# Optimization experiments

Measured on AMD Instinct MI355X. Metric: run time of the kernel, lower is better.

Reference implementation:

```python
import jax, jax.numpy as jnp
import numpy as np

N = 50000          # nodes
E = 800000         # edges (avg degree 16)
IN, HID, OUT = 128, 128, 32
BN_EPS = 1e-5


def gcn_conv(x, W, b, src, dst):
    """PyG GCNConv: D^-1/2 (A+I) D^-1/2 (x @ W) + b, self-loops included."""
    h = x @ W                                                  # [N, out]
    ones = jnp.ones((src.shape[0],), dtype=x.dtype)
    deg = jax.ops.segment_sum(ones, dst, num_segments=N) + 1.0  # in-degree + self-loop
    dis = jax.lax.rsqrt(deg)                                    # deg^-1/2
    norm = dis[src] * dis[dst]                                  # [E]
    msg = h[src] * norm[:, None]                                # gather + scale, [E, out]
    agg = jax.ops.segment_sum(msg, dst, num_segments=N)         # scatter-add
    agg = agg + h * (dis * dis)[:, None]                        # self-loop term (norm = 1/deg_i)
    return agg + b


def bn_relu(h, g, be):
    # BatchNorm1d in training mode: batch statistics over the node dimension
    mu = jnp.mean(h, axis=0)
    var = jnp.mean((h - mu) ** 2, axis=0)  # biased variance, as torch BN
    return jax.nn.relu((h - mu) * jax.lax.rsqrt(var + BN_EPS) * g + be)


def setup_inputs() -> dict:
    key = jax.random.key(0)
    ks = jax.random.split(key, 8)
    x = jax.random.normal(ks[0], (N, IN), dtype=jnp.float32)
    edge_index = jax.random.randint(ks[1], (2, E), 0, N, dtype=jnp.int64)
    W0 = jax.random.normal(ks[2], (IN, HID), dtype=jnp.float32) / np.sqrt(IN)
    W1 = jax.random.normal(ks[3], (HID, HID), dtype=jnp.float32) / np.sqrt(HID)
    W2 = jax.random.normal(ks[4], (HID, OUT), dtype=jnp.float32) / np.sqrt(HID)
    return {
        "x": x, "edge_index": edge_index,
        "W0": W0, "b0": jnp.zeros((HID,), jnp.float32),
        "g0": jnp.ones((HID,), jnp.float32), "be0": jnp.zeros((HID,), jnp.float32),
        "W1": W1, "b1": jnp.zeros((HID,), jnp.float32),
        "g1": jnp.ones((HID,), jnp.float32), "be1": jnp.zeros((HID,), jnp.float32),
        "W2": W2, "b2": jnp.zeros((OUT,), jnp.float32),
    }


def reference(x, edge_index, W0, b0, g0, be0, W1, b1, g1, be1, W2, b2):
    src, dst = edge_index[0], edge_index[1]
    # block 0: conv -> BN -> ReLU -> (dropout: eval, identity) -> residual
    h = bn_relu(gcn_conv(x, W0, b0, src, dst), g0, be0)
    x = h + x  # use_residual, in_channels == hidden, res_proj is None
    # block 1
    h = bn_relu(gcn_conv(x, W1, b1, src, dst), g1, be1)
    x = h + x
    # final conv + log_softmax over classes
    out = gcn_conv(x, W2, b2, src, dst)
    return jax.nn.log_softmax(out, axis=1)
```

## Files before the change

### kernel.cpp

```cpp
#include <hip/hip_runtime.h>
#include <math.h>

#define NN 50000
#define NNP (NN + 1)
#define NE 800000
#define NEP 1150000
#define NBLK 49
#define NBKT 7
#define BCAP 262144
#define GEMMBLK 782
#define FILLBLK 512

typedef __attribute__((ext_vector_type(8))) short short8;
typedef __attribute__((ext_vector_type(4))) float float4v;

__device__ inline unsigned int f2bf(float f) {
  unsigned int u = __float_as_uint(f);
  return (u + 0x7fffu + ((u >> 16) & 1u)) >> 16;
}
__device__ inline unsigned int pack2bf(float lo, float hi) {
  return f2bf(lo) | (f2bf(hi) << 16);
}
__device__ inline float bflo(unsigned int p) { return __uint_as_float(p << 16); }
__device__ inline float bfhi(unsigned int p) { return __uint_as_float(p & 0xffff0000u); }

__device__ inline void bn_fold(const float* __restrict__ gstat, const float* __restrict__ g,
                               const float* __restrict__ be, float* __restrict__ bnabS, int tid) {
  if (tid < 128) {
    float s = 0.f, q = 0.f;
    #pragma unroll
    for (int r = 0; r < 8; r++) {
      s += gstat[r * 256 + tid];
      q += gstat[r * 256 + 128 + tid];
    }
    const float inv = 1.f / (float)NN;
    float m = s * inv;
    float var = q * inv - m * m;
    float a = rsqrtf(var + 1e-5f) * g[tid];
    bnabS[tid] = a;
    bnabS[128 + tid] = be[tid] - m * a;
  }
}


__global__ __launch_bounds__(256) void k_init(int* __restrict__ deg, float* __restrict__ gstat,
                                              int* __restrict__ binCnt,
                                              const float* __restrict__ W0, const float* __restrict__ W1,
                                              const float* __restrict__ W2,
                                              unsigned short* __restrict__ wt16) {
  int i = blockIdx.x * 256 + threadIdx.x;
  if (i < NN) deg[i] = 0;
  if (i < 4096) gstat[i] = 0.f;
  if (i < NBKT) binCnt[i] = 0;
  if (i < 32768) {
    int w = i >> 14;
    int rem = i & 16383;
    int k = rem >> 7;
    int n = rem & 127;
    const float* W = w ? W1 : W0;
    wt16[w * 16384 + n * 128 + k] = (unsigned short)f2bf(W[k * 128 + n]);
  } else if (i < 36864) {
    int idx = i - 32768;
    int n = idx >> 7;
    int k = idx & 127;
    wt16[32768 + n * 128 + k] = (unsigned short)f2bf(W2[k * 32 + n]);
  }
}


__global__ __launch_bounds__(1024) void k_binA(const int* __restrict__ src, const int* __restrict__ dst,
                                               int* __restrict__ deg, int* __restrict__ binCnt,
                                               int2* __restrict__ bin) {
  __shared__ int lcnt[NBKT], lbase[NBKT];
  int tid = threadIdx.x;
  if (tid < NBKT) lcnt[tid] = 0;
  __syncthreads();
  int e = blockIdx.x * 1024 + tid;
  bool act = e < NE;
  int d = 0, s = 0, b = 0, rank = 0, drank = 0;
  if (act) {
    d = dst[e]; s = src[e];
    b = d >> 13;
    drank = atomicAdd(&deg[d], 1);
    rank = atomicAdd(&lcnt[b], 1);
  }
  __syncthreads();
  if (tid < NBKT && lcnt[tid] > 0) lbase[tid] = atomicAdd(&binCnt[tid], lcnt[tid]);
  __syncthreads();
  if (act) bin[(size_t)b * BCAP + lbase[b] + rank] =
      make_int2((int)((unsigned)d | ((unsigned)drank << 16)), s);
}


__global__ __launch_bounds__(1024) void k_scan1(const int* __restrict__ deg, int* __restrict__ degtot,
                                                int* __restrict__ excl, int* __restrict__ blksum) {
  __shared__ int smW[16];
  int t = threadIdx.x;
  int i = blockIdx.x * 1024 + t;
  int wv = t >> 6, ln = t & 63;
  int tot = 0;
  if (i < NN) {
    tot = deg[i];
    degtot[i] = tot;
  }
  int v = (i < NN) ? ((tot + 7) & ~7) : 0;
  int sc = v;
  #pragma unroll
  for (int off = 1; off < 64; off <<= 1) {
    int u = __shfl_up(sc, off);
    if (ln >= off) sc += u;
  }
  if (ln == 63) smW[wv] = sc;
  __syncthreads();
  if (t < 64) {
    int wsum = (t < 16) ? smW[t] : 0;
    int s2 = wsum;
    #pragma unroll
    for (int off = 1; off < 16; off <<= 1) {
      int u = __shfl_up(s2, off);
      if (t >= off) s2 += u;
    }
    if (t < 16) smW[t] = s2 - wsum;
    if (t == 15) blksum[blockIdx.x] = s2;
  }
  __syncthreads();
  if (i < NN) excl[i] = (sc - v) + smW[wv];
}


__global__ __launch_bounds__(256) void k_scan3(int* __restrict__ rowstart, const int* __restrict__ blksum,
                                               const int* __restrict__ degtot,
                                               float* __restrict__ dis,
                                               unsigned short* __restrict__ hs16, float* __restrict__ h2) {
  __shared__ int offS;
  int tid = threadIdx.x;
  int i = blockIdx.x * 256 + tid;
  int myblk = blockIdx.x >> 2;
  if (tid < 64) {
    int bv = (tid < NBLK) ? blksum[tid] : 0;
    int sc = bv;
    #pragma unroll
    for (int off = 1; off < 64; off <<= 1) {
      int u = __shfl_up(sc, off);
      if (tid >= off) sc += u;
    }
    int pre = (myblk > 0) ? __shfl(sc, myblk - 1) : 0;
    int total = __shfl(sc, NBLK - 1);
    if (tid == 0) {
      offS = pre;
      if (blockIdx.x == 0) rowstart[NN] = total;
    }
  }
  __syncthreads();
  int boff = offS;
  if (i < NN) {
    rowstart[i] = rowstart[i] + boff;
    dis[i] = rsqrtf((float)degtot[i] + 1.0f);
  }
  if (i < 64) {
    int slice = i >> 5, c = i & 31;
    ((unsigned int*)(hs16 + (size_t)slice * ((size_t)NNP * 64) + (size_t)NN * 64))[c] = 0u;
  }
  if (i < 32) h2[(size_t)NN * 32 + i] = 0.f;
}


__global__ __launch_bounds__(256) void k_fillgemm(const int2* __restrict__ bin,
                                                  const int* __restrict__ binCnt,
                                                  const int* __restrict__ rowstart,
                                                  int* __restrict__ csr_src,
                                                  const float* __restrict__ X,
                                                  const unsigned short* __restrict__ Wt,
                                                  const float* __restrict__ dis,
                                                  unsigned short* __restrict__ hs16) {
  __shared__ char smem[52224];
  const int tid = threadIdx.x;

  if (blockIdx.x < FILLBLK) {
    int bb = blockIdx.x;
    int b = bb & 7;
    if (b >= NBKT) return;
    int q = bb >> 3;
    int cnt = binCnt[b];
    const int2* __restrict__ B = bin + (size_t)b * BCAP;
    for (int i = q * 256 + tid; i < cnt; i += 64 * 256) {
      int2 ds = B[i];
      unsigned int v = (unsigned int)ds.x;
      int d = (int)(v & 0xffffu);
      int rank = (int)(v >> 16);
      csr_src[rowstart[d] + rank] = ds.y;
    }
    return;
  }

  unsigned short* A  = (unsigned short*)smem;
  unsigned short* Bt = (unsigned short*)(smem + 17408);
  float* C = (float*)smem;
  const int row0 = (blockIdx.x - FILLBLK) * 64;
  const int M = NN;

  {
    int c4 = tid & 31;
    #pragma unroll
    for (int i = 0; i < 8; i++) {
      int r = (tid >> 5) + i * 8;
      int gr = row0 + r;
      float4 v = make_float4(0.f, 0.f, 0.f, 0.f);
      if (gr < M) v = *(const float4*)(X + (size_t)gr * 128 + c4 * 4);
      *(uint2*)(A + r * 136 + c4 * 4) = make_uint2(pack2bf(v.x, v.y), pack2bf(v.z, v.w));
    }
  }
  {
    int r = tid >> 1, h = (tid & 1) * 64;
    const uint4* src = (const uint4*)(Wt + r * 128 + h);
    uint4* dst = (uint4*)(Bt + r * 136 + h);
    #pragma unroll
    for (int i = 0; i < 8; i++) dst[i] = src[i];
  }
  __syncthreads();

  const int wv = tid >> 6;
  const int l = tid & 63;
  const int lm = l & 15;
  const int lq = l >> 4;

  float4v acc[8];
  #pragma unroll
  for (int j = 0; j < 8; j++) acc[j] = (float4v)(0.f);

  const unsigned short* Arow = A + (wv * 16 + lm) * 136 + lq * 8;
  #pragma unroll
  for (int ks = 0; ks < 4; ks++) {
    short8 af = *(const short8*)(Arow + ks * 32);
    #pragma unroll
    for (int j = 0; j < 8; j++) {
      short8 bf = *(const short8*)(Bt + (j * 16 + lm) * 136 + lq * 8 + ks * 32);
      acc[j] = __builtin_amdgcn_mfma_f32_16x16x32_bf16(af, bf, acc[j], 0, 0, 0);
    }
  }
  __syncthreads();

  #pragma unroll
  for (int j = 0; j < 8; j++) {
    int col = j * 16 + lm;
    int rbase = wv * 16 + lq * 4;
    #pragma unroll
    for (int r = 0; r < 4; r++) C[(rbase + r) * 132 + col] = acc[j][r];
  }
  __syncthreads();

  {
    #pragma unroll
    for (int i = 0; i < 4; i++) {
      int idx = tid + i * 256;
      int slice = idx >> 9;
      int r = (idx >> 3) & 63;
      int ch = idx & 7;
      int gr = row0 + r;
      if (gr < M) {
        float d = dis[gr];
        const float* cp = C + r * 132 + slice * 64 + ch * 8;
        uint4 u;
        u.x = pack2bf(cp[0] * d, cp[1] * d);
        u.y = pack2bf(cp[2] * d, cp[3] * d);
        u.z = pack2bf(cp[4] * d, cp[5] * d);
        u.w = pack2bf(cp[6] * d, cp[7] * d);
        *(uint4*)(hs16 + (size_t)slice * ((size_t)NNP * 64) + (size_t)gr * 64 + ch * 8) = u;
      }
    }
  }
}


__global__ __launch_bounds__(256) void k_gemm128f(const unsigned short* __restrict__ O16,
                                                  const float* __restrict__ Xin,
                                                  unsigned short* __restrict__ XA16,
                                                  const float* __restrict__ gstat,
                                                  const float* __restrict__ g,
                                                  const float* __restrict__ be,
                                                  const unsigned short* __restrict__ Wt,
                                                  const float* __restrict__ dis,
                                                  unsigned short* __restrict__ hs16, int M) {
  __shared__ char smem[52224];
  __shared__ float bnabS[256];
  unsigned short* A  = (unsigned short*)smem;
  unsigned short* Bt = (unsigned short*)(smem + 17408);
  float* C = (float*)smem;
  const int tid = threadIdx.x;
  const int row0 = blockIdx.x * 64;

  bn_fold(gstat, g, be, bnabS, tid);
  __syncthreads();

  {
    int c = tid & 15;
    float4 alo = *(const float4*)(bnabS + c * 8);
    float4 ahi = *(const float4*)(bnabS + c * 8 + 4);
    float4 clo = *(const float4*)(bnabS + 128 + c * 8);
    float4 chi = *(const float4*)(bnabS + 128 + c * 8 + 4);
    #pragma unroll
    for (int i = 0; i < 4; i++) {
      int r = (tid >> 4) + i * 16;
      int gr = row0 + r;
      uint4 u = make_uint4(0u, 0u, 0u, 0u);
      if (gr < M) {
        uint4 ou = *(const uint4*)(O16 + (size_t)gr * 128 + c * 8);
        float4 xlo = *(const float4*)(Xin + (size_t)gr * 128 + c * 8);
        float4 xhi = *(const float4*)(Xin + (size_t)gr * 128 + c * 8 + 4);
        float v0 = fmaxf(bflo(ou.x) * alo.x + clo.x, 0.f) + xlo.x;
        float v1 = fmaxf(bfhi(ou.x) * alo.y + clo.y, 0.f) + xlo.y;
        float v2 = fmaxf(bflo(ou.y) * alo.z + clo.z, 0.f) + xlo.z;
        float v3 = fmaxf(bfhi(ou.y) * alo.w + clo.w, 0.f) + xlo.w;
        float v4 = fmaxf(bflo(ou.z) * ahi.x + chi.x, 0.f) + xhi.x;
        float v5 = fmaxf(bfhi(ou.z) * ahi.y + chi.y, 0.f) + xhi.y;
        float v6 = fmaxf(bflo(ou.w) * ahi.z + chi.z, 0.f) + xhi.z;
        float v7 = fmaxf(bfhi(ou.w) * ahi.w + chi.w, 0.f) + xhi.w;
        u.x = pack2bf(v0, v1);
        u.y = pack2bf(v2, v3);
        u.z = pack2bf(v4, v5);
        u.w = pack2bf(v6, v7);
        *(uint4*)(XA16 + (size_t)gr * 128 + c * 8) = u;
      }
      *(uint4*)(A + r * 136 + c * 8) = u;
    }
  }
  {
    int r = tid >> 1, h = (tid & 1) * 64;
    const uint4* src = (const uint4*)(Wt + r * 128 + h);
    uint4* dst = (uint4*)(Bt + r * 136 + h);
    #pragma unroll
    for (int i = 0; i < 8; i++) dst[i] = src[i];
  }
  __syncthreads();

  const int wv = tid >> 6;
  const int l = tid & 63;
  const int lm = l & 15;
  const int lq = l >> 4;

  float4v acc[8];
  #pragma unroll
  for (int j = 0; j < 8; j++) acc[j] = (float4v)(0.f);

  const unsigned short* Arow = A + (wv * 16 + lm) * 136 + lq * 8;
  #pragma unroll
  for (int ks = 0; ks < 4; ks++) {
    short8 af = *(const short8*)(Arow + ks * 32);
    #pragma unroll
    for (int j = 0; j < 8; j++) {
      short8 bf = *(const short8*)(Bt + (j * 16 + lm) * 136 + lq * 8 + ks * 32);
      acc[j] = __builtin_amdgcn_mfma_f32_16x16x32_bf16(af, bf, acc[j], 0, 0, 0);
    }
  }
  __syncthreads();

  #pragma unroll
  for (int j = 0; j < 8; j++) {
    int col = j * 16 + lm;
    int rbase = wv * 16 + lq * 4;
    #pragma unroll
    for (int r = 0; r < 4; r++) C[(rbase + r) * 132 + col] = acc[j][r];
  }
  __syncthreads();

  {
    #pragma unroll
    for (int i = 0; i < 4; i++) {
      int idx = tid + i * 256;
      int slice = idx >> 9;
      int r = (idx >> 3) & 63;
      int ch = idx & 7;
      int gr = row0 + r;
      if (gr < M) {
        float d = dis[gr];
        const float* cp = C + r * 132 + slice * 64 + ch * 8;
        uint4 u;
        u.x = pack2bf(cp[0] * d, cp[1] * d);
        u.y = pack2bf(cp[2] * d, cp[3] * d);
        u.z = pack2bf(cp[4] * d, cp[5] * d);
        u.w = pack2bf(cp[6] * d, cp[7] * d);
        *(uint4*)(hs16 + (size_t)slice * ((size_t)NNP * 64) + (size_t)gr * 64 + ch * 8) = u;
      }
    }
  }
}


__global__ __launch_bounds__(256) void k_gemm32mf(const unsigned short* __restrict__ O16,
                                                  const unsigned short* __restrict__ XA16,
                                                  const float* __restrict__ gstat,
                                                  const float* __restrict__ g,
                                                  const float* __restrict__ be,
                                                  const unsigned short* __restrict__ Wt2,
                                                  const float* __restrict__ dis,
                                                  float* __restrict__ H, int M) {
  __shared__ char smem[26112];
  __shared__ float bnabS[256];
  unsigned short* A   = (unsigned short*)smem;
  unsigned short* Bt2 = (unsigned short*)(smem + 17408);
  float* C = (float*)smem;
  const int tid = threadIdx.x;
  const int row0 = blockIdx.x * 64;

  bn_fold(gstat, g, be, bnabS, tid);
  __syncthreads();

  {
    int c = tid & 15;
    float4 alo = *(const float4*)(bnabS + c * 8);
    float4 ahi = *(const float4*)(bnabS + c * 8 + 4);
    float4 clo = *(const float4*)(bnabS + 128 + c * 8);
    float4 chi = *(const float4*)(bnabS + 128 + c * 8 + 4);
    #pragma unroll
    for (int i = 0; i < 4; i++) {
      int r = (tid >> 4) + i * 16;
      int gr = row0 + r;
      uint4 u = make_uint4(0u, 0u, 0u, 0u);
      if (gr < M) {
        uint4 ou = *(const uint4*)(O16 + (size_t)gr * 128 + c * 8);
        uint4 xu = *(const uint4*)(XA16 + (size_t)gr * 128 + c * 8);
        float v0 = fmaxf(bflo(ou.x) * alo.x + clo.x, 0.f) + bflo(xu.x);
        float v1 = fmaxf(bfhi(ou.x) * alo.y + clo.y, 0.f) + bfhi(xu.x);
        float v2 = fmaxf(bflo(ou.y) * alo.z + clo.z, 0.f) + bflo(xu.y);
        float v3 = fmaxf(bfhi(ou.y) * alo.w + clo.w, 0.f) + bfhi(xu.y);
        float v4 = fmaxf(bflo(ou.z) * ahi.x + chi.x, 0.f) + bflo(xu.z);
        float v5 = fmaxf(bfhi(ou.z) * ahi.y + chi.y, 0.f) + bfhi(xu.z);
        float v6 = fmaxf(bflo(ou.w) * ahi.z + chi.z, 0.f) + bflo(xu.w);
        float v7 = fmaxf(bfhi(ou.w) * ahi.w + chi.w, 0.f) + bfhi(xu.w);
        u.x = pack2bf(v0, v1);
        u.y = pack2bf(v2, v3);
        u.z = pack2bf(v4, v5);
        u.w = pack2bf(v6, v7);
      }
      *(uint4*)(A + r * 136 + c * 8) = u;
    }
  }
  {
    int r = tid >> 3, h = (tid & 7) * 16;
    const uint4* src = (const uint4*)(Wt2 + r * 128 + h);
    uint4* dst = (uint4*)(Bt2 + r * 136 + h);
    dst[0] = src[0];
    dst[1] = src[1];
  }
  __syncthreads();

  const int wv = tid >> 6;
  const int l = tid & 63;
  const int lm = l & 15;
  const int lq = l >> 4;

  float4v acc[2];
  acc[0] = (float4v)(0.f);
  acc[1] = (float4v)(0.f);

  const unsigned short* Arow = A + (wv * 16 + lm) * 136 + lq * 8;
  #pragma unroll
  for (int ks = 0; ks < 4; ks++) {
    short8 af = *(const short8*)(Arow + ks * 32);
    #pragma unroll
    for (int j = 0; j < 2; j++) {
      short8 bf = *(const short8*)(Bt2 + (j * 16 + lm) * 136 + lq * 8 + ks * 32);
      acc[j] = __builtin_amdgcn_mfma_f32_16x16x32_bf16(af, bf, acc[j], 0, 0, 0);
    }
  }
  __syncthreads();

  #pragma unroll
  for (int j = 0; j < 2; j++) {
    int col = j * 16 + lm;
    int rbase = wv * 16 + lq * 4;
    #pragma unroll
    for (int r = 0; r < 4; r++) C[(rbase + r) * 36 + col] = acc[j][r];
  }
  __syncthreads();

  {
    #pragma unroll
    for (int i = 0; i < 2; i++) {
      int idx = tid + i * 256;
      int r = idx >> 3;
      int ch = idx & 7;
      int gr = row0 + r;
      if (gr < M) {
        float d = dis[gr];
        const float* cp = C + r * 36 + ch * 4;
        float4 v = make_float4(cp[0] * d, cp[1] * d, cp[2] * d, cp[3] * d);
        *(float4*)(H + (size_t)gr * 32 + ch * 4) = v;
      }
    }
  }
}


__global__ __launch_bounds__(256) void k_agg128s(const unsigned short* __restrict__ Hs,
                                                 const float* __restrict__ dis,
                                                 const int* __restrict__ rowstart,
                                                 const int* __restrict__ degtot,
                                                 const int* __restrict__ csr_src,
                                                 const float* __restrict__ bias,
                                                 unsigned short* __restrict__ out16,
                                                 float* __restrict__ gstat) {
  __shared__ float smS[4][128], smQ[4][128];
  const int tid = threadIdx.x;
  const int wv = tid >> 6;
  const int lane = tid & 63;
  const int node_sub = lane >> 3;
  const int fl = lane & 7;
  const int base = node_sub * 8;
  const int w = blockIdx.x * 32 + wv * 8 + node_sub;
  const bool act = w < NN;
  const unsigned short* __restrict__ S0 = Hs + fl * 8;
  const unsigned short* __restrict__ S1 = Hs + (size_t)NNP * 64 + fl * 8;
  float di = act ? dis[w] : 0.f;
  int e0 = 0, e1 = 0, dend = 0;
  if (act) { e0 = rowstart[w]; e1 = rowstart[w + 1]; dend = e0 + degtot[w]; }

  float a0[8], a1[8];
  #pragma unroll
  for (int j = 0; j < 8; j++) { a0[j] = 0.f; a1[j] = 0.f; }

  int idxCur = (e0 < e1) ? csr_src[e0 + fl] : 0;
  for (int e = e0; e < e1; e += 8) {
    int cur = (e + fl < dend) ? idxCur : (int)NN;
    if (e + 8 < e1) idxCur = csr_src[e + 8 + fl];
    int s0 = __shfl(cur, base + 0), s1 = __shfl(cur, base + 1);
    int s2 = __shfl(cur, base + 2), s3 = __shfl(cur, base + 3);
    int s4 = __shfl(cur, base + 4), s5 = __shfl(cur, base + 5);
    int s6 = __shfl(cur, base + 6), s7 = __shfl(cur, base + 7);
    uint4 g0 = *(const uint4*)(S0 + (size_t)s0 * 64);
    uint4 g1 = *(const uint4*)(S0 + (size_t)s1 * 64);
    uint4 g2 = *(const uint4*)(S0 + (size_t)s2 * 64);
    uint4 g3 = *(const uint4*)(S0 + (size_t)s3 * 64);
    uint4 g4 = *(const uint4*)(S0 + (size_t)s4 * 64);
    uint4 g5 = *(const uint4*)(S0 + (size_t)s5 * 64);
    uint4 g6 = *(const uint4*)(S0 + (size_t)s6 * 64);
    uint4 g7 = *(const uint4*)(S0 + (size_t)s7 * 64);
    uint4 h0 = *(const uint4*)(S1 + (size_t)s0 * 64);
    uint4 h1 = *(const uint4*)(S1 + (size_t)s1 * 64);
    uint4 h2 = *(const uint4*)(S1 + (size_t)s2 * 64);
    uint4 h3 = *(const uint4*)(S1 + (size_t)s3 * 64);
    uint4 h4 = *(const uint4*)(S1 + (size_t)s4 * 64);
    uint4 h5 = *(const uint4*)(S1 + (size_t)s5 * 64);
    uint4 h6 = *(const uint4*)(S1 + (size_t)s6 * 64);
    uint4 h7 = *(const uint4*)(S1 + (size_t)s7 * 64);
    a0[0] += ((bflo(g0.x) + bflo(g1.x)) + (bflo(g2.x) + bflo(g3.x))) + ((bflo(g4.x) + bflo(g5.x)) + (bflo(g6.x) + bflo(g7.x)));
    a0[1] += ((bfhi(g0.x) + bfhi(g1.x)) + (bfhi(g2.x) + bfhi(g3.x))) + ((bfhi(g4.x) + bfhi(g5.x)) + (bfhi(g6.x) + bfhi(g7.x)));
    a0[2] += ((bflo(g0.y) + bflo(g1.y)) + (bflo(g2.y) + bflo(g3.y))) + ((bflo(g4.y) + bflo(g5.y)) + (bflo(g6.y) + bflo(g7.y)));
    a0[3] += ((bfhi(g0.y) + bfhi(g1.y)) + (bfhi(g2.y) + bfhi(g3.y))) + ((bfhi(g4.y) + bfhi(g5.y)) + (bfhi(g6.y) + bfhi(g7.y)));
    a0[4] += ((bflo(g0.z) + bflo(g1.z)) + (bflo(g2.z) + bflo(g3.z))) + ((bflo(g4.z) + bflo(g5.z)) + (bflo(g6.z) + bflo(g7.z)));
    a0[5] += ((bfhi(g0.z) + bfhi(g1.z)) + (bfhi(g2.z) + bfhi(g3.z))) + ((bfhi(g4.z) + bfhi(g5.z)) + (bfhi(g6.z) + bfhi(g7.z)));
    a0[6] += ((bflo(g0.w) + bflo(g1.w)) + (bflo(g2.w) + bflo(g3.w))) + ((bflo(g4.w) + bflo(g5.w)) + (bflo(g6.w) + bflo(g7.w)));
    a0[7] += ((bfhi(g0.w) + bfhi(g1.w)) + (bfhi(g2.w) + bfhi(g3.w))) + ((bfhi(g4.w) + bfhi(g5.w)) + (bfhi(g6.w) + bfhi(g7.w)));
    a1[0] += ((bflo(h0.x) + bflo(h1.x)) + (bflo(h2.x) + bflo(h3.x))) + ((bflo(h4.x) + bflo(h5.x)) + (bflo(h6.x) + bflo(h7.x)));
    a1[1] += ((bfhi(h0.x) + bfhi(h1.x)) + (bfhi(h2.x) + bfhi(h3.x))) + ((bfhi(h4.x) + bfhi(h5.x)) + (bfhi(h6.x) + bfhi(h7.x)));
    a1[2] += ((bflo(h0.y) + bflo(h1.y)) + (bflo(h2.y) + bflo(h3.y))) + ((bflo(h4.y) + bflo(h5.y)) + (bflo(h6.y) + bflo(h7.y)));
    a1[3] += ((bfhi(h0.y) + bfhi(h1.y)) + (bfhi(h2.y) + bfhi(h3.y))) + ((bfhi(h4.y) + bfhi(h5.y)) + (bfhi(h6.y) + bfhi(h7.y)));
    a1[4] += ((bflo(h0.z) + bflo(h1.z)) + (bflo(h2.z) + bflo(h3.z))) + ((bflo(h4.z) + bflo(h5.z)) + (bflo(h6.z) + bflo(h7.z)));
    a1[5] += ((bfhi(h0.z) + bfhi(h1.z)) + (bfhi(h2.z) + bfhi(h3.z))) + ((bfhi(h4.z) + bfhi(h5.z)) + (bfhi(h6.z) + bfhi(h7.z)));
    a1[6] += ((bflo(h0.w) + bflo(h1.w)) + (bflo(h2.w) + bflo(h3.w))) + ((bflo(h4.w) + bflo(h5.w)) + (bflo(h6.w) + bflo(h7.w)));
    a1[7] += ((bfhi(h0.w) + bfhi(h1.w)) + (bfhi(h2.w) + bfhi(h3.w))) + ((bfhi(h4.w) + bfhi(h5.w)) + (bfhi(h6.w) + bfhi(h7.w)));
  }

  float rv0[8], rv1[8];
  if (act) {
    uint4 sv0 = *(const uint4*)(S0 + (size_t)w * 64);
    uint4 sv1 = *(const uint4*)(S1 + (size_t)w * 64);
    float se0[8] = { bflo(sv0.x), bfhi(sv0.x), bflo(sv0.y), bfhi(sv0.y),
                     bflo(sv0.z), bfhi(sv0.z), bflo(sv0.w), bfhi(sv0.w) };
    float se1[8] = { bflo(sv1.x), bfhi(sv1.x), bflo(sv1.y), bfhi(sv1.y),
                     bflo(sv1.z), bfhi(sv1.z), bflo(sv1.w), bfhi(sv1.w) };
    #pragma unroll
    for (int j = 0; j < 8; j++) {
      rv0[j] = (a0[j] + se0[j]) * di + bias[fl * 8 + j];
      rv1[j] = (a1[j] + se1[j]) * di + bias[64 + fl * 8 + j];
    }
    uint4 u0, u1;
    u0.x = pack2bf(rv0[0], rv0[1]); u0.y = pack2bf(rv0[2], rv0[3]);
    u0.z = pack2bf(rv0[4], rv0[5]); u0.w = pack2bf(rv0[6], rv0[7]);
    u1.x = pack2bf(rv1[0], rv1[1]); u1.y = pack2bf(rv1[2], rv1[3]);
    u1.z = pack2bf(rv1[4], rv1[5]); u1.w = pack2bf(rv1[6], rv1[7]);
    *(uint4*)(out16 + (size_t)w * 128 + fl * 8)      = u0;
    *(uint4*)(out16 + (size_t)w * 128 + 64 + fl * 8) = u1;
  } else {
    #pragma unroll
    for (int j = 0; j < 8; j++) { rv0[j] = 0.f; rv1[j] = 0.f; }
  }

  float q0[8], q1[8];
  #pragma unroll
  for (int j = 0; j < 8; j++) { q0[j] = rv0[j] * rv0[j]; q1[j] = rv1[j] * rv1[j]; }
  #pragma unroll
  for (int off = 8; off <= 32; off <<= 1) {
    #pragma unroll
    for (int j = 0; j < 8; j++) {
      rv0[j] += __shfl_xor(rv0[j], off);
      q0[j]  += __shfl_xor(q0[j], off);
      rv1[j] += __shfl_xor(rv1[j], off);
      q1[j]  += __shfl_xor(q1[j], off);
    }
  }
  if (node_sub == 0) {
    #pragma unroll
    for (int j = 0; j < 8; j++) {
      smS[wv][fl * 8 + j] = rv0[j];      smQ[wv][fl * 8 + j] = q0[j];
      smS[wv][64 + fl * 8 + j] = rv1[j]; smQ[wv][64 + fl * 8 + j] = q1[j];
    }
  }
  __syncthreads();
  if (tid < 128) {
    float s = (smS[0][tid] + smS[1][tid]) + (smS[2][tid] + smS[3][tid]);
    float q = (smQ[0][tid] + smQ[1][tid]) + (smQ[2][tid] + smQ[3][tid]);
    int rep = blockIdx.x & 7;
    atomicAdd(&gstat[rep * 256 + tid], s);
    atomicAdd(&gstat[rep * 256 + 128 + tid], q);
  }
}


__global__ __launch_bounds__(256) void k_agg32lsm(const float* __restrict__ H2,
                                                  const float* __restrict__ dis,
                                                  const int* __restrict__ rowstart,
                                                  const int* __restrict__ degtot,
                                                  const int* __restrict__ csr_src,
                                                  const float* __restrict__ bias,
                                                  float* __restrict__ out) {
  int wave = (blockIdx.x * 256 + threadIdx.x) >> 6;
  int lane = threadIdx.x & 63;
  int half = lane >> 5;
  int l = lane & 31;
  int hbase = half * 32;
  int w = wave * 2 + half;
  if (w >= NN) return;
  const float* __restrict__ S = H2 + l;
  float di = dis[w];
  int e0 = rowstart[w], e1 = rowstart[w + 1];
  int dend = e0 + degtot[w];
  float acc = 0.f;
  for (int e = e0; e < e1; e += 8) {
    int myIdx = csr_src[e + (l & 7)];
    if (e + (l & 7) >= dend) myIdx = NN;
    int s0 = __shfl(myIdx, hbase + 0), s1 = __shfl(myIdx, hbase + 1);
    int s2 = __shfl(myIdx, hbase + 2), s3 = __shfl(myIdx, hbase + 3);
    int s4 = __shfl(myIdx, hbase + 4), s5 = __shfl(myIdx, hbase + 5);
    int s6 = __shfl(myIdx, hbase + 6), s7 = __shfl(myIdx, hbase + 7);
    float h0 = S[(size_t)s0 * 32], h1 = S[(size_t)s1 * 32];
    float h2v = S[(size_t)s2 * 32], h3 = S[(size_t)s3 * 32];
    float h4 = S[(size_t)s4 * 32], h5 = S[(size_t)s5 * 32];
    float h6 = S[(size_t)s6 * 32], h7 = S[(size_t)s7 * 32];
    acc += ((h0 + h1) + (h2v + h3)) + ((h4 + h5) + (h6 + h7));
  }
  float v = (acc + S[(size_t)w * 32]) * di + bias[l];
  float m = v;
  #pragma unroll
  for (int off = 16; off >= 1; off >>= 1) m = fmaxf(m, __shfl_xor(m, off));
  float ex = expf(v - m);
  float s = ex;
  #pragma unroll
  for (int off = 16; off >= 1; off >>= 1) s += __shfl_xor(s, off);
  out[(size_t)w * 32 + l] = v - m - logf(s);
}


extern "C" void kernel_launch(void* const* d_in, const int* in_sizes, int n_in,
                              void* d_out, int out_size, void* d_ws, size_t ws_size,
                              hipStream_t stream) {
  const float* x   = (const float*)d_in[0];
  const int*   ei  = (const int*)d_in[1];
  const float* W0  = (const float*)d_in[2];
  const float* b0  = (const float*)d_in[3];
  const float* g0  = (const float*)d_in[4];
  const float* be0 = (const float*)d_in[5];
  const float* W1  = (const float*)d_in[6];
  const float* b1  = (const float*)d_in[7];
  const float* g1  = (const float*)d_in[8];
  const float* be1 = (const float*)d_in[9];
  const float* W2  = (const float*)d_in[10];
  const float* b2  = (const float*)d_in[11];
  float* out = (float*)d_out;
  const int* srcI = ei;
  const int* dstI = ei + NE;

  char* p = (char*)d_ws;
  auto take = [&](size_t bytes) { char* r = p; p += (bytes + 255) & ~(size_t)255; return (void*)r; };
  int*   deg      = (int*)take(NN * 4);
  int*   degtot   = (int*)take(NN * 4);
  int*   rowstart = (int*)take((NN + 1) * 4);
  int*   blksum   = (int*)take(64 * 4);
  int*   binCnt   = (int*)take(8 * 4);
  float* dis      = (float*)take(NN * 4);
  int*   csr      = (int*)take((size_t)NEP * 4);
  int2*  bin      = (int2*)take((size_t)NBKT * BCAP * 8);
  float* gstat    = (float*)take(4096 * 4);
  unsigned short* wt16 = (unsigned short*)take((2 * 16384 + 4096) * 2);
  unsigned short* hs16 = (unsigned short*)take((size_t)NNP * 128 * 2);
  unsigned short* o16  = (unsigned short*)take((size_t)NN * 128 * 2);
  unsigned short* xA16 = (unsigned short*)take((size_t)NN * 128 * 2);
  float* h2       = (float*)take((size_t)NNP * 32 * 4);

  k_init<<<(NN + 255) / 256, 256, 0, stream>>>(deg, gstat, binCnt, W0, W1, W2, wt16);
  k_binA<<<(NE + 1023) / 1024, 1024, 0, stream>>>(srcI, dstI, deg, binCnt, bin);
  k_scan1<<<NBLK, 1024, 0, stream>>>(deg, degtot, rowstart, blksum);
  k_scan3<<<(NN + 255) / 256, 256, 0, stream>>>(rowstart, blksum, degtot, dis, hs16, h2);

  const int aggGrid = (NN + 31) / 32;
  const int aggGrid32 = (NN + 7) / 8;

  k_fillgemm<<<FILLBLK + GEMMBLK, 256, 0, stream>>>(bin, binCnt, rowstart, csr, x, wt16, dis, hs16);
  k_agg128s<<<aggGrid, 256, 0, stream>>>(hs16, dis, rowstart, degtot, csr, b0, o16, gstat);

  k_gemm128f<<<(NN + 63) / 64, 256, 0, stream>>>(o16, x, xA16, gstat, g0, be0,
                                                 wt16 + 16384, dis, hs16, NN);
  k_agg128s<<<aggGrid, 256, 0, stream>>>(hs16, dis, rowstart, degtot, csr, b1, o16, gstat + 2048);

  k_gemm32mf<<<(NN + 63) / 64, 256, 0, stream>>>(o16, xA16, gstat + 2048, g1, be1,
                                                 wt16 + 32768, dis, h2, NN);
  k_agg32lsm<<<aggGrid32, 256, 0, stream>>>(h2, dis, rowstart, degtot, csr, b2, out);
}
```

Before: 259.2 us.

## Merge preprocessing kernels: memset init, fold weight convert into binning, single-pass scan

Replaces the init kernel with a hipMemsetAsync over one contiguous zeroed region and moves the weight bf16 transpose into the edge-binning kernel. The two scan kernels become a single kernel that uses a global atomic counter as a grid barrier across its 49 blocks before applying block offsets and computing dis. The fill partition is also rebalanced to 448 blocks using modulo 7 so no blocks idle. This cuts launch count and overhead, but the spin barrier assumes all 49 blocks are co-resident.

```diff
diff --git a/kernel.cpp b/kernel.cpp
--- a/kernel.cpp
+++ b/kernel.cpp
@@ -9,7 +9,7 @@
 #define NBKT 7
 #define BCAP 262144
 #define GEMMBLK 782
-#define FILLBLK 512
+#define FILLBLK 448
 
 typedef __attribute__((ext_vector_type(8))) short short8;
 typedef __attribute__((ext_vector_type(4))) float float4v;
@@ -43,37 +43,31 @@
 }
 
 
-__global__ __launch_bounds__(256) void k_init(int* __restrict__ deg, float* __restrict__ gstat,
-                                              int* __restrict__ binCnt,
-                                              const float* __restrict__ W0, const float* __restrict__ W1,
-                                              const float* __restrict__ W2,
-                                              unsigned short* __restrict__ wt16) {
-  int i = blockIdx.x * 256 + threadIdx.x;
-  if (i < NN) deg[i] = 0;
-  if (i < 4096) gstat[i] = 0.f;
-  if (i < NBKT) binCnt[i] = 0;
-  if (i < 32768) {
-    int w = i >> 14;
-    int rem = i & 16383;
+__global__ __launch_bounds__(1024) void k_binAW(const int* __restrict__ src, const int* __restrict__ dst,
+                                                int* __restrict__ deg, int* __restrict__ binCnt,
+                                                int2* __restrict__ bin,
+                                                const float* __restrict__ W0, const float* __restrict__ W1,
+                                                const float* __restrict__ W2,
+                                                unsigned short* __restrict__ wt16) {
+  __shared__ int lcnt[NBKT], lbase[NBKT];
+  int tid = threadIdx.x;
+  if (tid < NBKT) lcnt[tid] = 0;
+
+  int j = blockIdx.x * 1024 + tid;
+  if (j < 32768) {
+    int w = j >> 14;
+    int rem = j & 16383;
     int k = rem >> 7;
     int n = rem & 127;
     const float* W = w ? W1 : W0;
     wt16[w * 16384 + n * 128 + k] = (unsigned short)f2bf(W[k * 128 + n]);
-  } else if (i < 36864) {
-    int idx = i - 32768;
+  } else if (j < 36864) {
+    int idx = j - 32768;
     int n = idx >> 7;
     int k = idx & 127;
     wt16[32768 + n * 128 + k] = (unsigned short)f2bf(W2[k * 32 + n]);
   }
-}
-
-
-__global__ __launch_bounds__(1024) void k_binA(const int* __restrict__ src, const int* __restrict__ dst,
-                                               int* __restrict__ deg, int* __restrict__ binCnt,
-                                               int2* __restrict__ bin) {
-  __shared__ int lcnt[NBKT], lbase[NBKT];
-  int tid = threadIdx.x;
-  if (tid < NBKT) lcnt[tid] = 0;
+
   __syncthreads();
   int e = blockIdx.x * 1024 + tid;
   bool act = e < NE;
@@ -92,9 +86,13 @@
 }
 
 
-__global__ __launch_bounds__(1024) void k_scan1(const int* __restrict__ deg, int* __restrict__ degtot,
-                                                int* __restrict__ excl, int* __restrict__ blksum) {
+__global__ __launch_bounds__(1024) void k_scan(const int* __restrict__ deg, int* __restrict__ degtot,
+                                               int* __restrict__ rowstart, int* __restrict__ blksum,
+                                               int* __restrict__ syncCnt,
+                                               float* __restrict__ dis,
+                                               unsigned short* __restrict__ hs16, float* __restrict__ h2) {
   __shared__ int smW[16];
+  __shared__ int smB[2];
   int t = threadIdx.x;
   int i = blockIdx.x * 1024 + t;
   int wv = t >> 6, ln = t & 63;
@@ -121,47 +119,43 @@
       if (t >= off) s2 += u;
     }
     if (t < 16) smW[t] = s2 - wsum;
-    if (t == 15) blksum[blockIdx.x] = s2;
-  }
-  __syncthreads();
-  if (i < NN) excl[i] = (sc - v) + smW[wv];
-}
-
-
-__global__ __launch_bounds__(256) void k_scan3(int* __restrict__ rowstart, const int* __restrict__ blksum,
-                                               const int* __restrict__ degtot,
-                                               float* __restrict__ dis,
-                                               unsigned short* __restrict__ hs16, float* __restrict__ h2) {
-  __shared__ int offS;
-  int tid = threadIdx.x;
-  int i = blockIdx.x * 256 + tid;
-  int myblk = blockIdx.x >> 2;
-  if (tid < 64) {
-    int bv = (tid < NBLK) ? blksum[tid] : 0;
-    int sc = bv;
+    if (t == 15) atomicExch(&blksum[blockIdx.x], s2);
+  }
+  __syncthreads();
+  int excl = (sc - v) + smW[wv];
+
+  if (t == 0) {
+    atomicAdd(syncCnt, 1);
+    while (atomicAdd(syncCnt, 0) < NBLK) { }
+  }
+  __syncthreads();
+
+  if (t < 64) {
+    int bv = (t < NBLK) ? atomicAdd(&blksum[t], 0) : 0;
+    int sc2 = bv;
     #pragma unroll
     for (int off = 1; off < 64; off <<= 1) {
-      int u = __shfl_up(sc, off);
-      if (tid >= off) sc += u;
-    }
-    int pre = (myblk > 0) ? __shfl(sc, myblk - 1) : 0;
-    int total = __shfl(sc, NBLK - 1);
-    if (tid == 0) {
-      offS = pre;
-      if (blockIdx.x == 0) rowstart[NN] = total;
-    }
-  }
-  __syncthreads();
-  int boff = offS;
+      int u = __shfl_up(sc2, off);
+      if (t >= off) sc2 += u;
+    }
+    int pre = (blockIdx.x > 0) ? __shfl(sc2, blockIdx.x - 1) : 0;
+    int total = __shfl(sc2, NBLK - 1);
+    if (t == 0) { smB[0] = pre; smB[1] = total; }
+  }
+  __syncthreads();
+  int boff = smB[0];
   if (i < NN) {
-    rowstart[i] = rowstart[i] + boff;
-    dis[i] = rsqrtf((float)degtot[i] + 1.0f);
-  }
-  if (i < 64) {
-    int slice = i >> 5, c = i & 31;
-    ((unsigned int*)(hs16 + (size_t)slice * ((size_t)NNP * 64) + (size_t)NN * 64))[c] = 0u;
-  }
-  if (i < 32) h2[(size_t)NN * 32 + i] = 0.f;
+    rowstart[i] = excl + boff;
+    dis[i] = rsqrtf((float)tot + 1.0f);
+  }
+  if (blockIdx.x == 0) {
+    if (t == 0) rowstart[NN] = smB[1];
+    if (t < 64) {
+      int slice = t >> 5, c = t & 31;
+      ((unsigned int*)(hs16 + (size_t)slice * ((size_t)NNP * 64) + (size_t)NN * 64))[c] = 0u;
+    }
+    if (t < 32) h2[(size_t)NN * 32 + t] = 0.f;
+  }
 }
 
 
@@ -177,10 +171,8 @@
   const int tid = threadIdx.x;
 
   if (blockIdx.x < FILLBLK) {
-    int bb = blockIdx.x;
-    int b = bb & 7;
-    if (b >= NBKT) return;
-    int q = bb >> 3;
+    int b = blockIdx.x % NBKT;
+    int q = blockIdx.x / NBKT;
     int cnt = binCnt[b];
     const int2* __restrict__ B = bin + (size_t)b * BCAP;
     for (int i = q * 256 + tid; i < cnt; i += 64 * 256) {
@@ -682,25 +674,27 @@
 
   char* p = (char*)d_ws;
   auto take = [&](size_t bytes) { char* r = p; p += (bytes + 255) & ~(size_t)255; return (void*)r; };
-  int*   deg      = (int*)take(NN * 4);
+  char*  zb       = (char*)take(217088);
+  int*   deg      = (int*)zb;
+  int*   binCnt   = (int*)(zb + 200192);
+  float* gstat    = (float*)(zb + 200448);
+  int*   syncCnt  = (int*)(zb + 216832);
   int*   degtot   = (int*)take(NN * 4);
   int*   rowstart = (int*)take((NN + 1) * 4);
   int*   blksum   = (int*)take(64 * 4);
-  int*   binCnt   = (int*)take(8 * 4);
   float* dis      = (float*)take(NN * 4);
   int*   csr      = (int*)take((size_t)NEP * 4);
   int2*  bin      = (int2*)take((size_t)NBKT * BCAP * 8);
-  float* gstat    = (float*)take(4096 * 4);
   unsigned short* wt16 = (unsigned short*)take((2 * 16384 + 4096) * 2);
   unsigned short* hs16 = (unsigned short*)take((size_t)NNP * 128 * 2);
   unsigned short* o16  = (unsigned short*)take((size_t)NN * 128 * 2);
   unsigned short* xA16 = (unsigned short*)take((size_t)NN * 128 * 2);
   float* h2       = (float*)take((size_t)NNP * 32 * 4);
 
-  k_init<<<(NN + 255) / 256, 256, 0, stream>>>(deg, gstat, binCnt, W0, W1, W2, wt16);
-  k_binA<<<(NE + 1023) / 1024, 1024, 0, stream>>>(srcI, dstI, deg, binCnt, bin);
-  k_scan1<<<NBLK, 1024, 0, stream>>>(deg, degtot, rowstart, blksum);
-  k_scan3<<<(NN + 255) / 256, 256, 0, stream>>>(rowstart, blksum, degtot, dis, hs16, h2);
+  hipMemsetAsync(zb, 0, 217088, stream);
+  k_binAW<<<(NE + 1023) / 1024, 1024, 0, stream>>>(srcI, dstI, deg, binCnt, bin,
+                                                   W0, W1, W2, wt16);
+  k_scan<<<NBLK, 1024, 0, stream>>>(deg, degtot, rowstart, blksum, syncCnt, dis, hs16, h2);
 
   const int aggGrid = (NN + 31) / 32;
   const int aggGrid32 = (NN + 7) / 8;
```

Result: no change. 262.0 us (+1.1%).
